# Performance work log

Measured on AMD Instinct MI355X. Metric: run time of the kernel, lower is better.

Reference implementation:

```python
import jax, jax.numpy as jnp
import numpy as np

B, IMG, TXT, DIM, H, D = 1, 1024, 256, 1536, 24, 64
SCALE = 1.0  # control cross-attn scale


def _lin(x, w, b):
    return x @ w + b


def _heads(x):  # [B,S,DIM] -> [B,H,S,D]
    return jnp.swapaxes(x.reshape(x.shape[0], x.shape[1], H, D), 1, 2)


def _merge(x):  # [B,H,S,D] -> [B,S,DIM]
    return jnp.swapaxes(x, 1, 2).reshape(x.shape[0], x.shape[2], H * D)


def _sdpa(q, k, v):
    s = jnp.einsum('bhqd,bhkd->bhqk', q, k) * (1.0 / np.sqrt(D))
    return jnp.einsum('bhqk,bhkd->bhqd', jax.nn.softmax(s, axis=-1), v)


def _rope(x, pe):  # x: [B,H,S,D], pe: [1,1,S,D//2,2,2]
    xr = x.reshape(*x.shape[:-1], -1, 1, 2)  # [B,H,S,D/2,1,2]
    out = pe[..., 0] * xr[..., 0] + pe[..., 1] * xr[..., 1]  # [B,H,S,D/2,2]
    return out.reshape(x.shape)


def _forward(hidden_states, encoder_hidden_states, hidden_states_control,
             encoder_hidden_states_control, img_to_q_control, pe,
             a_q_w, a_q_b, a_k_w, a_k_b, a_v_w, a_v_b,
             a_addq_w, a_addq_b, a_addk_w, a_addk_b, a_addv_w, a_addv_b,
             a_out_w, a_out_b, a_addout_w, a_addout_b,
             c_q_w, c_q_b, c_k_w, c_k_b, c_v_w, c_v_b,
             c_addq_w, c_addq_b, c_addk_w, c_addk_b, c_addv_w, c_addv_b,
             c_out_w, c_out_b, c_addout_w, c_addout_b):
    img_len = hidden_states.shape[1]
    # ---- main joint attention stream (no RoPE, per original) ----
    q = jnp.concatenate([_heads(_lin(hidden_states, a_q_w, a_q_b)),
                         _heads(_lin(encoder_hidden_states, a_addq_w, a_addq_b))], axis=2)
    k = jnp.concatenate([_heads(_lin(hidden_states, a_k_w, a_k_b)),
                         _heads(_lin(encoder_hidden_states, a_addk_w, a_addk_b))], axis=2)
    v = jnp.concatenate([_heads(_lin(hidden_states, a_v_w, a_v_b)),
                         _heads(_lin(encoder_hidden_states, a_addv_w, a_addv_b))], axis=2)
    hs = _merge(_sdpa(q, k, v))
    hs, ehs = hs[:, :img_len], hs[:, img_len:]
    # ---- control joint attention stream (with RoPE) ----
    qc = jnp.concatenate([_heads(_lin(hidden_states_control, c_q_w, c_q_b)),
                          _heads(_lin(encoder_hidden_states_control, c_addq_w, c_addq_b))], axis=2)
    kc = jnp.concatenate([_heads(_lin(hidden_states_control, c_k_w, c_k_b)),
                          _heads(_lin(encoder_hidden_states_control, c_addk_w, c_addk_b))], axis=2)
    vc = jnp.concatenate([_heads(_lin(hidden_states_control, c_v_w, c_v_b)),
                          _heads(_lin(encoder_hidden_states_control, c_addv_w, c_addv_b))], axis=2)
    key_cross, value_cross = kc, vc  # saved BEFORE RoPE, per original
    hsc = _merge(_sdpa(_rope(qc, pe), _rope(kc, pe), vc))
    hsc, ehsc = hsc[:, :img_len], hsc[:, img_len:]
    # ---- cross attention: img query attends to control K/V ----
    q_cross = _rope(_heads(img_to_q_control), pe[:, :, :img_len])
    k_cross = _rope(key_cross, pe[:, :, :key_cross.shape[2]])
    cross = _merge(_sdpa(q_cross, k_cross, value_cross))
    hs = hs + SCALE * cross
    # ---- output projections (to_out[1] is dropout p=0 -> identity) ----
    hs = _lin(hs, a_out_w, a_out_b)
    ehs = _lin(ehs, a_addout_w, a_addout_b)
    hsc = _lin(hsc, c_out_w, c_out_b)
    ehsc = _lin(ehsc, c_addout_w, c_addout_b)
    return hs, ehs, hsc, ehsc


def setup_inputs() -> dict:
    key = jax.random.key(0)
    ki = iter(jax.random.split(key, 80))
    d = {}
    d['hidden_states'] = jax.random.normal(next(ki), (B, IMG, DIM), jnp.float32)
    d['encoder_hidden_states'] = jax.random.normal(next(ki), (B, TXT, DIM), jnp.float32)
    d['hidden_states_control'] = jax.random.normal(next(ki), (B, IMG, DIM), jnp.float32)
    d['encoder_hidden_states_control'] = jax.random.normal(next(ki), (B, TXT, DIM), jnp.float32)
    d['img_to_q_control'] = jax.random.normal(next(ki), (B, IMG, DIM), jnp.float32)
    # realistic rotary pe: [1,1,S,D/2,2,2] rotation matrices
    S = IMG + TXT
    pos = np.arange(S, dtype=np.float32)
    freqs = 1.0 / (10000.0 ** (np.arange(0, D, 2, dtype=np.float32) / D))  # [D/2]
    ang = pos[:, None] * freqs[None, :]  # [S, D/2]
    cos, sin = np.cos(ang), np.sin(ang)
    pe = np.stack([np.stack([cos, -sin], -1), np.stack([sin, cos], -1)], -2)  # [S,D/2,2,2]
    d['pe'] = jnp.asarray(pe)[None, None]
    for p in ('a', 'c'):
        for name in ('q', 'k', 'v', 'addq', 'addk', 'addv', 'out', 'addout'):
            d[f'{p}_{name}_w'] = jax.random.normal(next(ki), (DIM, DIM), jnp.float32) * 0.02
            d[f'{p}_{name}_b'] = jax.random.normal(next(ki), (DIM,), jnp.float32) * 0.01
    return d


def reference(hidden_states, encoder_hidden_states, hidden_states_control,
              encoder_hidden_states_control, img_to_q_control, pe,
              a_q_w, a_q_b, a_k_w, a_k_b, a_v_w, a_v_b,
              a_addq_w, a_addq_b, a_addk_w, a_addk_b, a_addv_w, a_addv_b,
              a_out_w, a_out_b, a_addout_w, a_addout_b,
              c_q_w, c_q_b, c_k_w, c_k_b, c_v_w, c_v_b,
              c_addq_w, c_addq_b, c_addk_w, c_addk_b, c_addv_w, c_addv_b,
              c_out_w, c_out_b, c_addout_w, c_addout_b):
    return _forward(hidden_states, encoder_hidden_states, hidden_states_control,
                    encoder_hidden_states_control, img_to_q_control, pe,
                    a_q_w, a_q_b, a_k_w, a_k_b, a_v_w, a_v_b,
                    a_addq_w, a_addq_b, a_addk_w, a_addk_b, a_addv_w, a_addv_b,
                    a_out_w, a_out_b, a_addout_w, a_addout_b,
                    c_q_w, c_q_b, c_k_w, c_k_b, c_v_w, c_v_b,
                    c_addq_w, c_addq_b, c_addk_w, c_addk_b, c_addv_w, c_addv_b,
                    c_out_w, c_out_b, c_addout_w, c_addout_b)
```

## Files before the change

kernel.cpp:

```cpp
#include <hip/hip_runtime.h>

#define DIM 1536
#define IMG 1024
#define TXT 256
#define SEQ 1280
#define NH 24
#define HD 64
#define SD ((size_t)SEQ * DIM)
#define IDSZ ((size_t)IMG * DIM)

typedef __attribute__((ext_vector_type(8))) short short8;
typedef __attribute__((ext_vector_type(4))) float f32x4;

__device__ __forceinline__ float bf2f(ushort u) {
    union { unsigned int i; float f; } v; v.i = ((unsigned int)u) << 16; return v.f;
}
__device__ __forceinline__ ushort f2bf(float f) {
    union { unsigned int i; float f; } v; v.f = f;
    unsigned int u = v.i;
    u += 0x7fffu + ((u >> 16) & 1u);
    return (ushort)(u >> 16);
}

__global__ __launch_bounds__(256) void detect_dtype(const void* __restrict__ p,
                                                    int* __restrict__ flag)
{
    __shared__ int cnt;
    if (threadIdx.x == 0) cnt = 0;
    __syncthreads();
    const ushort* u = (const ushort*)p;
    int local = 0;
    for (int i = threadIdx.x; i < 2048; i += 256) {
        ushort v = u[2 * i];
        int e = (v >> 7) & 0xFF;
        if (e >= 0xC0) local++;
    }
    atomicAdd(&cnt, local);
    __syncthreads();
    if (threadIdx.x == 0) flag[0] = (cnt > 16) ? 1 : 0;
}

#define LSTR 40


struct QKV2P {
    const void* Xi[2]; const void* Xt[2];
    const void* W[12];
    const void* B[12];
    float* Y[6];
    ushort* Yh[6];
    ushort* Yl[6];
};

__global__ __launch_bounds__(256) void gemm_qkv_v3(QKV2P p, const int* __restrict__ dflag)
{
    __shared__ __align__(16) ushort As[2][128 * LSTR];
    __shared__ __align__(16) ushort Bs[2][64 * 64];
    const int dt = dflag[0];
    const int bx = blockIdx.x;
    const int wsel = bx / 12;
    const int n0 = (bx - wsel * 12) * 128;
    const int ys = blockIdx.y;
    const int str = (ys >= 10) ? 1 : 0;
    const int m0g = (ys - str * 10) * 128;
    const bool istxt = (m0g >= IMG);
    const int m0 = istxt ? (m0g - IMG) : m0g;
    const void* X  = istxt ? p.Xt[str] : p.Xi[str];
    const int widx = str * 6 + wsel + (istxt ? 3 : 0);
    const void* Wp = p.W[widx];
    const void* Bp = p.B[widx];
    const int yidx = str * 3 + wsel;
    float*  Y  = p.Y[yidx];
    ushort* yh = p.Yh[yidx];
    ushort* yl = p.Yl[yidx];

    const int t = threadIdx.x;
    const int wave = t >> 6, lane = t & 63;
    const int quad = lane >> 4, l16 = lane & 15;
    const int wm = (wave >> 1) * 64, wn = (wave & 1) * 64;

    const int arow = t >> 1, apair = t & 1;
    const int bn8 = (t & 15) << 3, bkk = (t >> 4) << 1;
    const int aps = apair ^ ((arow >> 3) & 1);
    const int adst = arow * LSTR + aps * 16;
    const int bkg = bkk >> 3, bo = bkk & 7;

    f32x4 acc[4][4];
#pragma unroll
    for (int i = 0; i < 4; ++i)
#pragma unroll
        for (int j = 0; j < 4; ++j) acc[i][j] = (f32x4)(0.0f);

    float4 raf[4]; uint4 rau[2];
    float4 rbf[4]; uint4 rbu[2];

    auto loadA = [&](int k0) {
        const size_t off = (size_t)(m0 + arow) * DIM + k0 + apair * 16;
        if (dt) {
            const float* xp = (const float*)X + off;
            raf[0] = *(const float4*)xp;       raf[1] = *(const float4*)(xp + 4);
            raf[2] = *(const float4*)(xp + 8); raf[3] = *(const float4*)(xp + 12);
        } else {
            const ushort* xp = (const ushort*)X + off;
            rau[0] = *(const uint4*)xp;
            rau[1] = *(const uint4*)(xp + 8);
        }
    };
    auto loadB = [&](int k0) {
        const size_t off = (size_t)(k0 + bkk) * DIM + n0 + bn8;
        if (dt) {
            const float* wp0 = (const float*)Wp + off;
            rbf[0] = *(const float4*)wp0;         rbf[1] = *(const float4*)(wp0 + 4);
            rbf[2] = *(const float4*)(wp0 + DIM); rbf[3] = *(const float4*)(wp0 + DIM + 4);
        } else {
            const ushort* wp0 = (const ushort*)Wp + off;
            rbu[0] = *(const uint4*)wp0;
            rbu[1] = *(const uint4*)(wp0 + DIM);
        }
    };
    auto storeA = [&](int buf) {
        ushort tmp[16];
        if (dt) {
            const float* xs = (const float*)raf;
#pragma unroll
            for (int i = 0; i < 16; ++i) tmp[i] = f2bf(xs[i]);
        } else {
            *(uint4*)&tmp[0] = rau[0];
            *(uint4*)&tmp[8] = rau[1];
        }
        *(uint4*)&As[buf][adst]     = *(uint4*)&tmp[0];
        *(uint4*)&As[buf][adst + 8] = *(uint4*)&tmp[8];
    };
    auto storeB = [&](int buf) {
        ushort t0[8], t1[8];
        if (dt) {
            const float* f = (const float*)rbf;
#pragma unroll
            for (int j = 0; j < 8; ++j) { t0[j] = f2bf(f[j]); t1[j] = f2bf(f[8 + j]); }
        } else {
            *(uint4*)t0 = rbu[0];
            *(uint4*)t1 = rbu[1];
        }
#pragma unroll
        for (int j = 0; j < 8; ++j) {
            const int rr = bn8 + j;
            const int R = rr & 63, half = rr >> 6;
            const int gx = (((half << 2) + bkg) ^ (R & 7) ^ (R >> 3)) & 7;
            *(unsigned int*)&Bs[buf][R * 64 + gx * 8 + bo] =
                (unsigned int)t0[j] | ((unsigned int)t1[j] << 16);
        }
    };

    loadA(0); loadB(0);
    storeA(0); storeB(0);
    __syncthreads();

    for (int k = 0; k < DIM / 32; ++k) {
        const int cur = k & 1;
        const bool hn = (k + 1) < DIM / 32;
        if (hn) { loadA((k + 1) * 32); loadB((k + 1) * 32); }

        short8 b[4];
#pragma unroll
        for (int j = 0; j < 4; ++j) {
            const int rrn = wn + j * 16 + l16;
            const int R = rrn & 63, half = rrn >> 6;
            const int gx = (((half << 2) + quad) ^ (R & 7) ^ (R >> 3)) & 7;
            b[j] = *(const short8*)&Bs[cur][R * 64 + gx * 8];
        }
#pragma unroll
        for (int i = 0; i < 4; ++i) {
            const int rr = wm + i * 16 + l16;
            const int ps = (quad >> 1) ^ ((rr >> 3) & 1);
            const int col = ps * 16 + (quad & 1) * 8;
            short8 a = *(const short8*)&As[cur][rr * LSTR + col];
#pragma unroll
            for (int j = 0; j < 4; ++j)
                acc[i][j] = __builtin_amdgcn_mfma_f32_16x16x32_bf16(a, b[j], acc[i][j], 0, 0, 0);
        }
        if (hn) { storeA(cur ^ 1); storeB(cur ^ 1); }
        __syncthreads();
    }

#pragma unroll
    for (int j = 0; j < 4; ++j) {
        const int col = n0 + wn + j * 16 + l16;
        const float bv = dt ? ((const float*)Bp)[col] : bf2f(((const ushort*)Bp)[col]);
#pragma unroll
        for (int i = 0; i < 4; ++i)
#pragma unroll
            for (int r = 0; r < 4; ++r) {
                const int row = m0g + wm + i * 16 + quad * 4 + r;
                const size_t o = (size_t)row * DIM + col;
                const float val = acc[i][j][r] + bv;
                if (Y) Y[o] = val;
                if (yh) {
                    const ushort hv = f2bf(val);
                    yh[o] = hv;
                    yl[o] = f2bf(val - bf2f(hv));
                }
            }
    }
}

struct OutP {
    const float* X;
    const void* W[4]; const void* B[4];
    void* out;
};

__global__ __launch_bounds__(256) void gemm_out_v3(OutP p, const int* __restrict__ dflag)
{
    __shared__ __align__(16) ushort Ah[2][64 * LSTR];
    __shared__ __align__(16) ushort Al[2][64 * LSTR];
    __shared__ __align__(16) ushort Bs[2][64 * 64];
    const int dt = dflag[0];
    const int n0 = blockIdx.x * 128;
    const int mt = blockIdx.y;
    const int seg = (mt < 16) ? 0 : (mt < 20) ? 1 : (mt < 36) ? 2 : 3;
    const void* Wp = p.W[seg];
    const void* Bp = p.B[seg];
    const int m0 = mt * 64;

    const int t = threadIdx.x;
    const int wave = t >> 6, lane = t & 63;
    const int quad = lane >> 4, l16 = lane & 15;
    const int wm = (wave >> 1) * 32, wn = (wave & 1) * 64;

    const int arow = t >> 2, ag = t & 3;
    const int apg = ag >> 1, asub = ag & 1;
    const int aps = apg ^ ((arow >> 3) & 1);
    const int adst = arow * LSTR + aps * 16 + asub * 8;
    const int bn8 = (t & 15) << 3, bkk = (t >> 4) << 1;
    const int bkg = bkk >> 3, bo = bkk & 7;

    f32x4 acc[2][4];
#pragma unroll
    for (int i = 0; i < 2; ++i)
#pragma unroll
        for (int j = 0; j < 4; ++j) acc[i][j] = (f32x4)(0.0f);

    float4 raf[2];
    float4 rbf[4]; uint4 rbu[2];

    auto loadA = [&](int k0) {
        const float* xp = p.X + (size_t)(m0 + arow) * DIM + k0 + ag * 8;
        raf[0] = *(const float4*)xp;
        raf[1] = *(const float4*)(xp + 4);
    };
    auto loadB = [&](int k0) {
        const size_t off = (size_t)(k0 + bkk) * DIM + n0 + bn8;
        if (dt) {
            const float* wp0 = (const float*)Wp + off;
            rbf[0] = *(const float4*)wp0;         rbf[1] = *(const float4*)(wp0 + 4);
            rbf[2] = *(const float4*)(wp0 + DIM); rbf[3] = *(const float4*)(wp0 + DIM + 4);
        } else {
            const ushort* wp0 = (const ushort*)Wp + off;
            rbu[0] = *(const uint4*)wp0;
            rbu[1] = *(const uint4*)(wp0 + DIM);
        }
    };
    auto storeA = [&](int buf) {
        ushort hi[8], lo[8];
        const float* xs = (const float*)raf;
#pragma unroll
        for (int i = 0; i < 8; ++i) {
            hi[i] = f2bf(xs[i]);
            lo[i] = f2bf(xs[i] - bf2f(hi[i]));
        }
        *(uint4*)&Ah[buf][adst] = *(uint4*)&hi[0];
        *(uint4*)&Al[buf][adst] = *(uint4*)&lo[0];
    };
    auto storeB = [&](int buf) {
        ushort t0[8], t1[8];
        if (dt) {
            const float* f = (const float*)rbf;
#pragma unroll
            for (int j = 0; j < 8; ++j) { t0[j] = f2bf(f[j]); t1[j] = f2bf(f[8 + j]); }
        } else {
            *(uint4*)t0 = rbu[0];
            *(uint4*)t1 = rbu[1];
        }
#pragma unroll
        for (int j = 0; j < 8; ++j) {
            const int rr = bn8 + j;
            const int R = rr & 63, half = rr >> 6;
            const int gx = (((half << 2) + bkg) ^ (R & 7) ^ (R >> 3)) & 7;
            *(unsigned int*)&Bs[buf][R * 64 + gx * 8 + bo] =
                (unsigned int)t0[j] | ((unsigned int)t1[j] << 16);
        }
    };

    loadA(0); loadB(0);
    storeA(0); storeB(0);
    __syncthreads();

    for (int k = 0; k < DIM / 32; ++k) {
        const int cur = k & 1;
        const bool hn = (k + 1) < DIM / 32;
        if (hn) { loadA((k + 1) * 32); loadB((k + 1) * 32); }

        short8 b[4];
#pragma unroll
        for (int j = 0; j < 4; ++j) {
            const int rrn = wn + j * 16 + l16;
            const int R = rrn & 63, half = rrn >> 6;
            const int gx = (((half << 2) + quad) ^ (R & 7) ^ (R >> 3)) & 7;
            b[j] = *(const short8*)&Bs[cur][R * 64 + gx * 8];
        }
#pragma unroll
        for (int i = 0; i < 2; ++i) {
            const int rr = wm + i * 16 + l16;
            const int ps = (quad >> 1) ^ ((rr >> 3) & 1);
            const int col = ps * 16 + (quad & 1) * 8;
            short8 ah = *(const short8*)&Ah[cur][rr * LSTR + col];
            short8 al = *(const short8*)&Al[cur][rr * LSTR + col];
#pragma unroll
            for (int j = 0; j < 4; ++j) {
                acc[i][j] = __builtin_amdgcn_mfma_f32_16x16x32_bf16(ah, b[j], acc[i][j], 0, 0, 0);
                acc[i][j] = __builtin_amdgcn_mfma_f32_16x16x32_bf16(al, b[j], acc[i][j], 0, 0, 0);
            }
        }
        if (hn) { storeA(cur ^ 1); storeB(cur ^ 1); }
        __syncthreads();
    }

#pragma unroll
    for (int j = 0; j < 4; ++j) {
        const int col = n0 + wn + j * 16 + l16;
        const float bv = dt ? ((const float*)Bp)[col] : bf2f(((const ushort*)Bp)[col]);
#pragma unroll
        for (int i = 0; i < 2; ++i)
#pragma unroll
            for (int r = 0; r < 4; ++r) {
                const int grow = m0 + wm + i * 16 + quad * 4 + r;
                const size_t o = (size_t)grow * DIM + col;
                const float val = acc[i][j][r] + bv;
                if (dt) ((float*)p.out)[o] = val;
                else    ((ushort*)p.out)[o] = f2bf(val);
            }
    }
}

__device__ __forceinline__ void pe_load(const void* pe, int dt, size_t off,
                                        float& c00, float& c01, float& c10, float& c11)
{
    if (dt) {
        float4 pv = *(const float4*)((const float*)pe + off);
        c00 = pv.x; c01 = pv.y; c10 = pv.z; c11 = pv.w;
    } else {
        const ushort* pp = (const ushort*)pe + off;
        c00 = bf2f(pp[0]); c01 = bf2f(pp[1]); c10 = bf2f(pp[2]); c11 = bf2f(pp[3]);
    }
}

__global__ __launch_bounds__(256) void rope_f32_to_split(
    const float* __restrict__ src, const void* __restrict__ pe,
    ushort* __restrict__ dh, ushort* __restrict__ dl,
    const int* __restrict__ dflag, int S)
{
    const int dt = dflag[0];
    int idx = blockIdx.x * 256 + threadIdx.x;
    if (idx >= S * 768) return;
    int s = idx / 768, pp = idx - s * 768;
    int col = pp << 1, i = pp & 31;
    float2 xv = *(const float2*)(src + (size_t)s * DIM + col);
    float c00, c01, c10, c11;
    pe_load(pe, dt, (size_t)s * 128 + i * 4, c00, c01, c10, c11);
    float y0 = c00 * xv.x + c01 * xv.y;
    float y1 = c10 * xv.x + c11 * xv.y;
    ushort h0 = f2bf(y0), h1 = f2bf(y1);
    ushort l0 = f2bf(y0 - bf2f(h0)), l1 = f2bf(y1 - bf2f(h1));
    *(unsigned int*)(dh + (size_t)s * DIM + col) = (unsigned int)h0 | ((unsigned int)h1 << 16);
    *(unsigned int*)(dl + (size_t)s * DIM + col) = (unsigned int)l0 | ((unsigned int)l1 << 16);
}

__global__ __launch_bounds__(256) void rope_in_to_split(
    const void* __restrict__ src, const void* __restrict__ pe,
    ushort* __restrict__ dh, ushort* __restrict__ dl,
    const int* __restrict__ dflag, int S)
{
    const int dt = dflag[0];
    int idx = blockIdx.x * 256 + threadIdx.x;
    if (idx >= S * 768) return;
    int s = idx / 768, pp = idx - s * 768;
    int col = pp << 1, i = pp & 31;
    float x0, x1;
    if (dt) {
        float2 xv = *(const float2*)((const float*)src + (size_t)s * DIM + col);
        x0 = xv.x; x1 = xv.y;
    } else {
        const ushort* sp = (const ushort*)src + (size_t)s * DIM + col;
        x0 = bf2f(sp[0]); x1 = bf2f(sp[1]);
    }
    float c00, c01, c10, c11;
    pe_load(pe, dt, (size_t)s * 128 + i * 4, c00, c01, c10, c11);
    float y0 = c00 * x0 + c01 * x1;
    float y1 = c10 * x0 + c11 * x1;
    ushort h0 = f2bf(y0), h1 = f2bf(y1);
    ushort l0 = f2bf(y0 - bf2f(h0)), l1 = f2bf(y1 - bf2f(h1));
    *(unsigned int*)(dh + (size_t)s * DIM + col) = (unsigned int)h0 | ((unsigned int)h1 << 16);
    *(unsigned int*)(dl + (size_t)s * DIM + col) = (unsigned int)l0 | ((unsigned int)l1 << 16);
}

__global__ __launch_bounds__(256) void vtrans_split(
    const float* __restrict__ V, ushort* __restrict__ Vth, ushort* __restrict__ Vtl,
    int seq)
{
    __shared__ unsigned int tile[64 * 65];
    const int s0 = blockIdx.x * 64;
    const int h = blockIdx.y;
    const int t = threadIdx.x;
#pragma unroll
    for (int it = 0; it < 16; ++it) {
        const int sl = (t >> 6) + (it << 2);
        const int d = t & 63;
        const float v = V[(size_t)(s0 + sl) * DIM + h * HD + d];
        const ushort hv = f2bf(v);
        const ushort lv = f2bf(v - bf2f(hv));
        tile[d * 65 + sl] = (unsigned int)hv | ((unsigned int)lv << 16);
    }
    __syncthreads();
    const int d = t >> 2, cc = (t & 3) << 4;
    ushort th[16], tl[16];
#pragma unroll
    for (int j = 0; j < 16; ++j) {
        const unsigned int w = tile[d * 65 + cc + j];
        th[j] = (ushort)w;
        tl[j] = (ushort)(w >> 16);
    }
    const size_t off = (size_t)(h * HD + d) * seq + s0 + cc;
    *(uint4*)(Vth + off)     = *(uint4*)&th[0];
    *(uint4*)(Vth + off + 8) = *(uint4*)&th[8];
    *(uint4*)(Vtl + off)     = *(uint4*)&tl[0];
    *(uint4*)(Vtl + off + 8) = *(uint4*)&tl[8];
}

__device__ __forceinline__ int swz(int row, int col) {
    return row * 64 + ((((col >> 3) ^ row) & 7) << 3) + (col & 7);
}
__device__ __forceinline__ short8 ldfrag(const ushort* plane, int row, int col) {
    return *(const short8*)&plane[swz(row, col)];
}

struct AttnP {
    const ushort *Qh, *Ql, *Kh, *Kl, *Vth, *Vtl;
    float* Op0;
    float* Op1;
    float2* Ml;
    int kvchunk;
    int kvstride;
};

__global__ __launch_bounds__(256) void attn_mfma_split(AttnP p)
{
    __shared__ ushort Qh_[4096], Ql_[4096];
    __shared__ ushort Kh_[4096], Kl_[4096];
    __shared__ ushort Vh_[4096], Vl_[4096];

    const int q0 = blockIdx.x * 64;
    const int h = blockIdx.y;
    const int z = blockIdx.z;
    const int t = threadIdx.x;
    const int wave = t >> 6, lane = t & 63;
    const int quad = lane >> 4, l16 = lane & 15;
    const int wq0 = wave * 16;

    const int srow = t >> 2, c0 = (t & 3) << 4;
    const int g0 = c0 >> 3;
    const int p0 = ((g0 ^ (srow & 7)) & 7) << 3;
    const int p1 = (((g0 + 1) ^ (srow & 7)) & 7) << 3;

    {
        const size_t off = (size_t)(q0 + srow) * DIM + h * HD + c0;
        *(uint4*)&Qh_[srow * 64 + p0] = *(const uint4*)(p.Qh + off);
        *(uint4*)&Qh_[srow * 64 + p1] = *(const uint4*)(p.Qh + off + 8);
        *(uint4*)&Ql_[srow * 64 + p0] = *(const uint4*)(p.Ql + off);
        *(uint4*)&Ql_[srow * 64 + p1] = *(const uint4*)(p.Ql + off + 8);
    }
    short8 qfh[2], qfl[2];
#pragma unroll
    for (int c = 0; c < 2; ++c) {
        qfh[c] = ldfrag(Qh_, wq0 + l16, c * 32 + quad * 8);
        qfl[c] = ldfrag(Ql_, wq0 + l16, c * 32 + quad * 8);
    }

    float m_[4], l_[4];
#pragma unroll
    for (int r = 0; r < 4; ++r) { m_[r] = -3e38f; l_[r] = 0.0f; }
    f32x4 Oacc[4];
#pragma unroll
    for (int j = 0; j < 4; ++j) Oacc[j] = (f32x4)(0.0f);

    const int kvbeg = z * p.kvchunk;
    for (int kt = 0; kt < p.kvchunk; kt += 64) {
        const int kv0 = kvbeg + kt;
        __syncthreads();
        {
            const size_t off = (size_t)(kv0 + srow) * DIM + h * HD + c0;
            *(uint4*)&Kh_[srow * 64 + p0] = *(const uint4*)(p.Kh + off);
            *(uint4*)&Kh_[srow * 64 + p1] = *(const uint4*)(p.Kh + off + 8);
            *(uint4*)&Kl_[srow * 64 + p0] = *(const uint4*)(p.Kl + off);
            *(uint4*)&Kl_[srow * 64 + p1] = *(const uint4*)(p.Kl + off + 8);
        }
        {
            const size_t off = (size_t)(h * HD + srow) * p.kvstride + kv0 + c0;
            *(uint4*)&Vh_[srow * 64 + p0] = *(const uint4*)(p.Vth + off);
            *(uint4*)&Vh_[srow * 64 + p1] = *(const uint4*)(p.Vth + off + 8);
            *(uint4*)&Vl_[srow * 64 + p0] = *(const uint4*)(p.Vtl + off);
            *(uint4*)&Vl_[srow * 64 + p1] = *(const uint4*)(p.Vtl + off + 8);
        }
        __syncthreads();

        f32x4 S[4];
#pragma unroll
        for (int j = 0; j < 4; ++j) S[j] = (f32x4)(0.0f);
#pragma unroll
        for (int c = 0; c < 2; ++c) {
#pragma unroll
            for (int j = 0; j < 4; ++j) {
                short8 bh = ldfrag(Kh_, j * 16 + l16, c * 32 + quad * 8);
                short8 bl = ldfrag(Kl_, j * 16 + l16, c * 32 + quad * 8);
                S[j] = __builtin_amdgcn_mfma_f32_16x16x32_bf16(qfh[c], bh, S[j], 0, 0, 0);
                S[j] = __builtin_amdgcn_mfma_f32_16x16x32_bf16(qfl[c], bh, S[j], 0, 0, 0);
                S[j] = __builtin_amdgcn_mfma_f32_16x16x32_bf16(qfh[c], bl, S[j], 0, 0, 0);
            }
        }
#pragma unroll
        for (int j = 0; j < 4; ++j)
#pragma unroll
            for (int r = 0; r < 4; ++r) S[j][r] *= 0.125f;

        float alpha[4];
#pragma unroll
        for (int r = 0; r < 4; ++r) {
            float mx = fmaxf(fmaxf(S[0][r], S[1][r]), fmaxf(S[2][r], S[3][r]));
            mx = fmaxf(mx, __shfl_xor(mx, 1));
            mx = fmaxf(mx, __shfl_xor(mx, 2));
            mx = fmaxf(mx, __shfl_xor(mx, 4));
            mx = fmaxf(mx, __shfl_xor(mx, 8));
            float mn = fmaxf(m_[r], mx);
            alpha[r] = __expf(m_[r] - mn);
            m_[r] = mn;
            float rs = 0.0f;
#pragma unroll
            for (int j = 0; j < 4; ++j) {
                float pv = __expf(S[j][r] - mn);
                S[j][r] = pv;
                rs += pv;
            }
            rs += __shfl_xor(rs, 1);
            rs += __shfl_xor(rs, 2);
            rs += __shfl_xor(rs, 4);
            rs += __shfl_xor(rs, 8);
            l_[r] = l_[r] * alpha[r] + rs;
        }
#pragma unroll
        for (int j = 0; j < 4; ++j)
#pragma unroll
            for (int r = 0; r < 4; ++r) Oacc[j][r] *= alpha[r];

        {
            const int prow = wq0 + quad * 4;
#pragma unroll
            for (int j = 0; j < 4; ++j)
#pragma unroll
                for (int r = 0; r < 4; ++r) {
                    float pv = S[j][r];
                    ushort ph = f2bf(pv);
                    ushort pl = f2bf(pv - bf2f(ph));
                    int idx = swz(prow + r, j * 16 + l16);
                    Qh_[idx] = ph;
                    Ql_[idx] = pl;
                }
        }

#pragma unroll
        for (int c = 0; c < 2; ++c) {
            short8 pah = ldfrag(Qh_, wq0 + l16, c * 32 + quad * 8);
            short8 pal = ldfrag(Ql_, wq0 + l16, c * 32 + quad * 8);
#pragma unroll
            for (int jn = 0; jn < 4; ++jn) {
                short8 vbh = ldfrag(Vh_, jn * 16 + l16, c * 32 + quad * 8);
                short8 vbl = ldfrag(Vl_, jn * 16 + l16, c * 32 + quad * 8);
                Oacc[jn] = __builtin_amdgcn_mfma_f32_16x16x32_bf16(pah, vbh, Oacc[jn], 0, 0, 0);
                Oacc[jn] = __builtin_amdgcn_mfma_f32_16x16x32_bf16(pal, vbh, Oacc[jn], 0, 0, 0);
                Oacc[jn] = __builtin_amdgcn_mfma_f32_16x16x32_bf16(pah, vbl, Oacc[jn], 0, 0, 0);
            }
        }
    }

    float* Opz = z ? p.Op1 : p.Op0;
#pragma unroll
    for (int r = 0; r < 4; ++r) {
        const int rowq = q0 + wq0 + quad * 4 + r;
        if (l16 == 0)
            p.Ml[((size_t)z * NH + h) * SEQ + rowq] = make_float2(m_[r], l_[r]);
#pragma unroll
        for (int jn = 0; jn < 4; ++jn)
            Opz[(size_t)rowq * DIM + h * HD + jn * 16 + l16] = Oacc[jn][r];
    }
}

__global__ __launch_bounds__(256) void attn_merge(
    const float* __restrict__ Op0, const float* __restrict__ Op1,
    const float2* __restrict__ Ml,
    float* __restrict__ out, const float* __restrict__ addto, int qlen)
{
    const int idx = blockIdx.x * 256 + threadIdx.x;
    if (idx >= qlen * 384) return;
    const int rowq = idx / 384;
    const int c4 = (idx - rowq * 384) << 2;
    const float2 a = Ml[(size_t)(c4 >> 6) * SEQ + rowq];
    const float2 b = Ml[(size_t)(NH + (c4 >> 6)) * SEQ + rowq];
    const float ms = fmaxf(a.x, b.x);
    const float s0 = __expf(a.x - ms), s1 = __expf(b.x - ms);
    const float inv = 1.0f / (s0 * a.y + s1 * b.y);
    const float4 o0 = *(const float4*)&Op0[(size_t)rowq * DIM + c4];
    const float4 o1 = *(const float4*)&Op1[(size_t)rowq * DIM + c4];
    float4 r;
    r.x = (s0 * o0.x + s1 * o1.x) * inv;
    r.y = (s0 * o0.y + s1 * o1.y) * inv;
    r.z = (s0 * o0.z + s1 * o1.z) * inv;
    r.w = (s0 * o0.w + s1 * o1.w) * inv;
    if (addto) {
        const float4 c = *(const float4*)&addto[(size_t)rowq * DIM + c4];
        r.x += c.x; r.y += c.y; r.z += c.z; r.w += c.w;
    }
    *(float4*)&out[(size_t)rowq * DIM + c4] = r;
}

extern "C" void kernel_launch(void* const* d_in, const int* in_sizes, int n_in,
                              void* d_out, int out_size, void* d_ws, size_t ws_size,
                              hipStream_t stream) {
    (void)in_sizes; (void)n_in; (void)out_size; (void)ws_size;
    const void* hs   = d_in[0];
    const void* ehs  = d_in[1];
    const void* hsc  = d_in[2];
    const void* ehsc = d_in[3];
    const void* i2q  = d_in[4];
    const void* pe   = d_in[5];
#define W_(i) ((const void*)d_in[i])

    int*   flag = (int*)d_ws;
    float* fb = (float*)((char*)d_ws + 256);
    float* q1 = fb;
    float* k1 = q1 + SD;
    float* v1 = k1 + SD;
    float* vC = v1 + SD;
    float* oA = vC + SD;
    float* oC = oA + SD;
    ushort* qh  = (ushort*)(oC + SD);
    ushort* qlo = qh + SD;
    ushort* kh  = qlo + SD;
    ushort* klo = kh + SD;
    ushort* vth = klo + SD;
    ushort* vtl = vth + SD;
    ushort* qxh = vtl + SD;
    ushort* qxl = qxh + IDSZ;
    float2* Ml = (float2*)(qxl + IDSZ);

    dim3 blk(256);
    detect_dtype<<<1, blk, 0, stream>>>(hs, flag);

    QKV2P qp;
    qp.Xi[0] = hs;  qp.Xt[0] = ehs;
    qp.Xi[1] = hsc; qp.Xt[1] = ehsc;
    for (int j = 0; j < 3; ++j) {
        qp.W[j]     = W_(6 + 2 * j);   qp.B[j]     = W_(7 + 2 * j);
        qp.W[3 + j] = W_(12 + 2 * j);  qp.B[3 + j] = W_(13 + 2 * j);
        qp.W[6 + j] = W_(22 + 2 * j);  qp.B[6 + j] = W_(23 + 2 * j);
        qp.W[9 + j] = W_(28 + 2 * j);  qp.B[9 + j] = W_(29 + 2 * j);
    }
    for (int j = 0; j < 6; ++j) { qp.Y[j] = nullptr; qp.Yh[j] = nullptr; qp.Yl[j] = nullptr; }
    qp.Yh[0] = qh;  qp.Yl[0] = qlo;
    qp.Yh[1] = kh;  qp.Yl[1] = klo;
    qp.Y[2] = v1;
    qp.Y[3] = q1;
    qp.Y[4] = k1;
    qp.Y[5] = vC;
    gemm_qkv_v3<<<dim3(36, 20), blk, 0, stream>>>(qp, flag);

    auto ATTN = [&](const ushort* Qhp, const ushort* Qlp, int qblocks,
                    float* Op0, float* Op1) {
        AttnP p;
        p.Qh = Qhp; p.Ql = Qlp;
        p.Kh = kh;  p.Kl = klo;
        p.Vth = vth; p.Vtl = vtl;
        p.Op0 = Op0; p.Op1 = Op1; p.Ml = Ml;
        p.kvchunk = SEQ / 2; p.kvstride = SEQ;
        attn_mfma_split<<<dim3(qblocks, NH, 2), blk, 0, stream>>>(p);
    };

    vtrans_split<<<dim3(SEQ / 64, NH), blk, 0, stream>>>(v1, vth, vtl, SEQ);
    ATTN(qh, qlo, SEQ / 64, v1, oC);
    attn_merge<<<(SEQ * 384 + 255) / 256, blk, 0, stream>>>(v1, oC, Ml, oA, nullptr, SEQ);

    rope_f32_to_split<<<(SEQ * 768 + 255) / 256, blk, 0, stream>>>(q1, pe, qh, qlo, flag, SEQ);
    rope_f32_to_split<<<(SEQ * 768 + 255) / 256, blk, 0, stream>>>(k1, pe, kh, klo, flag, SEQ);
    rope_in_to_split<<<(IMG * 768 + 255) / 256, blk, 0, stream>>>(i2q, pe, qxh, qxl, flag, IMG);
    vtrans_split<<<dim3(SEQ / 64, NH), blk, 0, stream>>>(vC, vth, vtl, SEQ);

    ATTN(qh, qlo, SEQ / 64, v1, oC);
    attn_merge<<<(SEQ * 384 + 255) / 256, blk, 0, stream>>>(v1, oC, Ml, oC, nullptr, SEQ);

    ATTN(qxh, qxl, IMG / 64, v1, vC);
    attn_merge<<<(IMG * 384 + 255) / 256, blk, 0, stream>>>(v1, vC, Ml, oA, oA, IMG);

    OutP op;
    op.X = oA;
    op.W[0] = W_(18); op.B[0] = W_(19);
    op.W[1] = W_(20); op.B[1] = W_(21);
    op.W[2] = W_(34); op.B[2] = W_(35);
    op.W[3] = W_(36); op.B[3] = W_(37);
    op.out = d_out;
    gemm_out_v3<<<dim3(12, 40), blk, 0, stream>>>(op, flag);
#undef W_
}
```

Baseline: 682.5 us.

## Pre-convert QKV weights and inputs to bf16; split Q inside attention

Adds a single batched conversion kernel that writes all twelve QKV weight matrices and the four activation inputs as bf16 into workspace. The QKV GEMM then reads only bf16 and no longer carries per-tile fp32 loads and conversion. Q is now stored as fp32 and split into hi/lo bf16 inside the attention kernel when it is loaded, so the separate Q split buffers go away and rope on Q runs in place. The cost is an extra full pass over the weights, about 28 MB of added bf16 writes and later reads, plus reshuffled workspace aliasing and higher attention Q-load traffic.

After: 654.9 us. 4.0% less time.

```diff
diff --git a/kernel.cpp b/kernel.cpp
--- a/kernel.cpp
+++ b/kernel.cpp
@@ -8,6 +8,7 @@
 #define HD 64
 #define SD ((size_t)SEQ * DIM)
 #define IDSZ ((size_t)IMG * DIM)
+#define WSZ ((size_t)DIM * DIM)
 
 typedef __attribute__((ext_vector_type(8))) short short8;
 typedef __attribute__((ext_vector_type(4))) float f32x4;
@@ -40,19 +41,45 @@
     if (threadIdx.x == 0) flag[0] = (cnt > 16) ? 1 : 0;
 }
 
+struct CvtP {
+    const void* src[16];
+    ushort* dst[16];
+    int n8[16];
+};
+
+__global__ __launch_bounds__(256) void convert_bf16(CvtP p, const int* __restrict__ dflag)
+{
+    const int a = blockIdx.y;
+    const int i = blockIdx.x * 256 + threadIdx.x;
+    if (i >= p.n8[a]) return;
+    const size_t off = (size_t)i * 8;
+    uint4 o;
+    if (dflag[0]) {
+        const float* s = (const float*)p.src[a] + off;
+        const float4 f0 = *(const float4*)s;
+        const float4 f1 = *(const float4*)(s + 4);
+        ushort t[8];
+        t[0] = f2bf(f0.x); t[1] = f2bf(f0.y); t[2] = f2bf(f0.z); t[3] = f2bf(f0.w);
+        t[4] = f2bf(f1.x); t[5] = f2bf(f1.y); t[6] = f2bf(f1.z); t[7] = f2bf(f1.w);
+        o = *(uint4*)t;
+    } else {
+        o = *(const uint4*)((const ushort*)p.src[a] + off);
+    }
+    *(uint4*)(p.dst[a] + off) = o;
+}
+
 #define LSTR 40
 
-
-struct QKV2P {
-    const void* Xi[2]; const void* Xt[2];
-    const void* W[12];
+struct QKV3P {
+    const ushort* Xb;
+    const ushort* Wb;
     const void* B[12];
     float* Y[6];
     ushort* Yh[6];
     ushort* Yl[6];
 };
 
-__global__ __launch_bounds__(256) void gemm_qkv_v3(QKV2P p, const int* __restrict__ dflag)
+__global__ __launch_bounds__(256) void gemm_qkv_v4(QKV3P p, const int* __restrict__ dflag)
 {
     __shared__ __align__(16) ushort As[2][128 * LSTR];
     __shared__ __align__(16) ushort Bs[2][64 * 64];
@@ -64,10 +91,9 @@
     const int str = (ys >= 10) ? 1 : 0;
     const int m0g = (ys - str * 10) * 128;
     const bool istxt = (m0g >= IMG);
-    const int m0 = istxt ? (m0g - IMG) : m0g;
-    const void* X  = istxt ? p.Xt[str] : p.Xi[str];
     const int widx = str * 6 + wsel + (istxt ? 3 : 0);
-    const void* Wp = p.W[widx];
+    const ushort* X  = p.Xb + (size_t)str * SD;
+    const ushort* Wp = p.Wb + (size_t)widx * WSZ;
     const void* Bp = p.B[widx];
     const int yidx = str * 3 + wsel;
     float*  Y  = p.Y[yidx];
@@ -91,56 +117,27 @@
 #pragma unroll
         for (int j = 0; j < 4; ++j) acc[i][j] = (f32x4)(0.0f);
 
-    float4 raf[4]; uint4 rau[2];
-    float4 rbf[4]; uint4 rbu[2];
+    uint4 rau[2];
+    uint4 rbu[2];
 
     auto loadA = [&](int k0) {
-        const size_t off = (size_t)(m0 + arow) * DIM + k0 + apair * 16;
-        if (dt) {
-            const float* xp = (const float*)X + off;
-            raf[0] = *(const float4*)xp;       raf[1] = *(const float4*)(xp + 4);
-            raf[2] = *(const float4*)(xp + 8); raf[3] = *(const float4*)(xp + 12);
-        } else {
-            const ushort* xp = (const ushort*)X + off;
-            rau[0] = *(const uint4*)xp;
-            rau[1] = *(const uint4*)(xp + 8);
-        }
+        const ushort* xp = X + (size_t)(m0g + arow) * DIM + k0 + apair * 16;
+        rau[0] = *(const uint4*)xp;
+        rau[1] = *(const uint4*)(xp + 8);
     };
     auto loadB = [&](int k0) {
-        const size_t off = (size_t)(k0 + bkk) * DIM + n0 + bn8;
-        if (dt) {
-            const float* wp0 = (const float*)Wp + off;
-            rbf[0] = *(const float4*)wp0;         rbf[1] = *(const float4*)(wp0 + 4);
-            rbf[2] = *(const float4*)(wp0 + DIM); rbf[3] = *(const float4*)(wp0 + DIM + 4);
-        } else {
-            const ushort* wp0 = (const ushort*)Wp + off;
-            rbu[0] = *(const uint4*)wp0;
-            rbu[1] = *(const uint4*)(wp0 + DIM);
-        }
+        const ushort* wp0 = Wp + (size_t)(k0 + bkk) * DIM + n0 + bn8;
+        rbu[0] = *(const uint4*)wp0;
+        rbu[1] = *(const uint4*)(wp0 + DIM);
     };
     auto storeA = [&](int buf) {
-        ushort tmp[16];
-        if (dt) {
-            const float* xs = (const float*)raf;
-#pragma unroll
-            for (int i = 0; i < 16; ++i) tmp[i] = f2bf(xs[i]);
-        } else {
-            *(uint4*)&tmp[0] = rau[0];
-            *(uint4*)&tmp[8] = rau[1];
-        }
-        *(uint4*)&As[buf][adst]     = *(uint4*)&tmp[0];
-        *(uint4*)&As[buf][adst + 8] = *(uint4*)&tmp[8];
+        *(uint4*)&As[buf][adst]     = rau[0];
+        *(uint4*)&As[buf][adst + 8] = rau[1];
     };
     auto storeB = [&](int buf) {
         ushort t0[8], t1[8];
-        if (dt) {
-            const float* f = (const float*)rbf;
-#pragma unroll
-            for (int j = 0; j < 8; ++j) { t0[j] = f2bf(f[j]); t1[j] = f2bf(f[8 + j]); }
-        } else {
-            *(uint4*)t0 = rbu[0];
-            *(uint4*)t1 = rbu[1];
-        }
+        *(uint4*)t0 = rbu[0];
+        *(uint4*)t1 = rbu[1];
 #pragma unroll
         for (int j = 0; j < 8; ++j) {
             const int rr = bn8 + j;
@@ -352,6 +349,23 @@
         const ushort* pp = (const ushort*)pe + off;
         c00 = bf2f(pp[0]); c01 = bf2f(pp[1]); c10 = bf2f(pp[2]); c11 = bf2f(pp[3]);
     }
+}
+
+__global__ __launch_bounds__(256) void rope_f32_inplace(
+    float* __restrict__ buf, const void* __restrict__ pe,
+    const int* __restrict__ dflag, int S)
+{
+    const int dt = dflag[0];
+    int idx = blockIdx.x * 256 + threadIdx.x;
+    if (idx >= S * 768) return;
+    int s = idx / 768, pp = idx - s * 768;
+    int col = pp << 1, i = pp & 31;
+    float* bp = buf + (size_t)s * DIM + col;
+    float x0 = bp[0], x1 = bp[1];
+    float c00, c01, c10, c11;
+    pe_load(pe, dt, (size_t)s * 128 + i * 4, c00, c01, c10, c11);
+    bp[0] = c00 * x0 + c01 * x1;
+    bp[1] = c10 * x0 + c11 * x1;
 }
 
 __global__ __launch_bounds__(256) void rope_f32_to_split(
@@ -375,10 +389,9 @@
     *(unsigned int*)(dl + (size_t)s * DIM + col) = (unsigned int)l0 | ((unsigned int)l1 << 16);
 }
 
-__global__ __launch_bounds__(256) void rope_in_to_split(
+__global__ __launch_bounds__(256) void rope_in_to_f32(
     const void* __restrict__ src, const void* __restrict__ pe,
-    ushort* __restrict__ dh, ushort* __restrict__ dl,
-    const int* __restrict__ dflag, int S)
+    float* __restrict__ dst, const int* __restrict__ dflag, int S)
 {
     const int dt = dflag[0];
     int idx = blockIdx.x * 256 + threadIdx.x;
@@ -395,12 +408,9 @@
     }
     float c00, c01, c10, c11;
     pe_load(pe, dt, (size_t)s * 128 + i * 4, c00, c01, c10, c11);
-    float y0 = c00 * x0 + c01 * x1;
-    float y1 = c10 * x0 + c11 * x1;
-    ushort h0 = f2bf(y0), h1 = f2bf(y1);
-    ushort l0 = f2bf(y0 - bf2f(h0)), l1 = f2bf(y1 - bf2f(h1));
-    *(unsigned int*)(dh + (size_t)s * DIM + col) = (unsigned int)h0 | ((unsigned int)h1 << 16);
-    *(unsigned int*)(dl + (size_t)s * DIM + col) = (unsigned int)l0 | ((unsigned int)l1 << 16);
+    float* dp = dst + (size_t)s * DIM + col;
+    dp[0] = c00 * x0 + c01 * x1;
+    dp[1] = c10 * x0 + c11 * x1;
 }
 
 __global__ __launch_bounds__(256) void vtrans_split(
@@ -444,7 +454,8 @@
 }
 
 struct AttnP {
-    const ushort *Qh, *Ql, *Kh, *Kl, *Vth, *Vtl;
+    const float* Qf;
+    const ushort *Kh, *Kl, *Vth, *Vtl;
     float* Op0;
     float* Op1;
     float2* Ml;
@@ -472,11 +483,22 @@
     const int p1 = (((g0 + 1) ^ (srow & 7)) & 7) << 3;
 
     {
-        const size_t off = (size_t)(q0 + srow) * DIM + h * HD + c0;
-        *(uint4*)&Qh_[srow * 64 + p0] = *(const uint4*)(p.Qh + off);
-        *(uint4*)&Qh_[srow * 64 + p1] = *(const uint4*)(p.Qh + off + 8);
-        *(uint4*)&Ql_[srow * 64 + p0] = *(const uint4*)(p.Ql + off);
-        *(uint4*)&Ql_[srow * 64 + p1] = *(const uint4*)(p.Ql + off + 8);
+        const float* src = p.Qf + (size_t)(q0 + srow) * DIM + h * HD + c0;
+        float x[16];
+        *(float4*)&x[0]  = *(const float4*)(src);
+        *(float4*)&x[4]  = *(const float4*)(src + 4);
+        *(float4*)&x[8]  = *(const float4*)(src + 8);
+        *(float4*)&x[12] = *(const float4*)(src + 12);
+        ushort hi[16], lo[16];
+#pragma unroll
+        for (int i = 0; i < 16; ++i) {
+            hi[i] = f2bf(x[i]);
+            lo[i] = f2bf(x[i] - bf2f(hi[i]));
+        }
+        *(uint4*)&Qh_[srow * 64 + p0] = *(uint4*)&hi[0];
+        *(uint4*)&Qh_[srow * 64 + p1] = *(uint4*)&hi[8];
+        *(uint4*)&Ql_[srow * 64 + p0] = *(uint4*)&lo[0];
+        *(uint4*)&Ql_[srow * 64 + p1] = *(uint4*)&lo[8];
     }
     short8 qfh[2], qfl[2];
 #pragma unroll
@@ -650,41 +672,53 @@
     float* vC = v1 + SD;
     float* oA = vC + SD;
     float* oC = oA + SD;
-    ushort* qh  = (ushort*)(oC + SD);
-    ushort* qlo = qh + SD;
-    ushort* kh  = qlo + SD;
+    ushort* kh  = (ushort*)(oC + SD);
     ushort* klo = kh + SD;
     ushort* vth = klo + SD;
     ushort* vtl = vth + SD;
-    ushort* qxh = vtl + SD;
-    ushort* qxl = qxh + IDSZ;
-    float2* Ml = (float2*)(qxl + IDSZ);
+    ushort* Wbf = vtl + SD;
+    ushort* Xbf = Wbf + 12 * WSZ;
+    float2* Ml = (float2*)(Xbf + 2 * SD);
+    float* qA = oC;
+    float* qx = k1;
 
     dim3 blk(256);
     detect_dtype<<<1, blk, 0, stream>>>(hs, flag);
 
-    QKV2P qp;
-    qp.Xi[0] = hs;  qp.Xt[0] = ehs;
-    qp.Xi[1] = hsc; qp.Xt[1] = ehsc;
-    for (int j = 0; j < 3; ++j) {
-        qp.W[j]     = W_(6 + 2 * j);   qp.B[j]     = W_(7 + 2 * j);
-        qp.W[3 + j] = W_(12 + 2 * j);  qp.B[3 + j] = W_(13 + 2 * j);
-        qp.W[6 + j] = W_(22 + 2 * j);  qp.B[6 + j] = W_(23 + 2 * j);
-        qp.W[9 + j] = W_(28 + 2 * j);  qp.B[9 + j] = W_(29 + 2 * j);
+    {
+        CvtP cp;
+        const int wsrc[12] = {6, 8, 10, 12, 14, 16, 22, 24, 26, 28, 30, 32};
+        for (int j = 0; j < 12; ++j) {
+            cp.src[j] = W_(wsrc[j]);
+            cp.dst[j] = Wbf + (size_t)j * WSZ;
+            cp.n8[j] = (int)(WSZ / 8);
+        }
+        cp.src[12] = hs;   cp.dst[12] = Xbf;                cp.n8[12] = (int)(IDSZ / 8);
+        cp.src[13] = ehs;  cp.dst[13] = Xbf + IDSZ;         cp.n8[13] = (int)((size_t)TXT * DIM / 8);
+        cp.src[14] = hsc;  cp.dst[14] = Xbf + SD;           cp.n8[14] = (int)(IDSZ / 8);
+        cp.src[15] = ehsc; cp.dst[15] = Xbf + SD + IDSZ;    cp.n8[15] = (int)((size_t)TXT * DIM / 8);
+        convert_bf16<<<dim3((int)(WSZ / 8 + 255) / 256, 16), blk, 0, stream>>>(cp, flag);
+    }
+
+    QKV3P qp;
+    qp.Xb = Xbf;
+    qp.Wb = Wbf;
+    {
+        const int bsrc[12] = {7, 9, 11, 13, 15, 17, 23, 25, 27, 29, 31, 33};
+        for (int j = 0; j < 12; ++j) qp.B[j] = W_(bsrc[j]);
     }
     for (int j = 0; j < 6; ++j) { qp.Y[j] = nullptr; qp.Yh[j] = nullptr; qp.Yl[j] = nullptr; }
-    qp.Yh[0] = qh;  qp.Yl[0] = qlo;
+    qp.Y[0] = qA;
     qp.Yh[1] = kh;  qp.Yl[1] = klo;
     qp.Y[2] = v1;
     qp.Y[3] = q1;
     qp.Y[4] = k1;
     qp.Y[5] = vC;
-    gemm_qkv_v3<<<dim3(36, 20), blk, 0, stream>>>(qp, flag);
-
-    auto ATTN = [&](const ushort* Qhp, const ushort* Qlp, int qblocks,
-                    float* Op0, float* Op1) {
+    gemm_qkv_v4<<<dim3(36, 20), blk, 0, stream>>>(qp, flag);
+
+    auto ATTN = [&](const float* Qfp, int qblocks, float* Op0, float* Op1) {
         AttnP p;
-        p.Qh = Qhp; p.Ql = Qlp;
+        p.Qf = Qfp;
         p.Kh = kh;  p.Kl = klo;
         p.Vth = vth; p.Vtl = vtl;
         p.Op0 = Op0; p.Op1 = Op1; p.Ml = Ml;
@@ -693,18 +727,18 @@
     };
 
     vtrans_split<<<dim3(SEQ / 64, NH), blk, 0, stream>>>(v1, vth, vtl, SEQ);
-    ATTN(qh, qlo, SEQ / 64, v1, oC);
-    attn_merge<<<(SEQ * 384 + 255) / 256, blk, 0, stream>>>(v1, oC, Ml, oA, nullptr, SEQ);
-
-    rope_f32_to_split<<<(SEQ * 768 + 255) / 256, blk, 0, stream>>>(q1, pe, qh, qlo, flag, SEQ);
+    ATTN(qA, SEQ / 64, v1, oA);
+    attn_merge<<<(SEQ * 384 + 255) / 256, blk, 0, stream>>>(v1, oA, Ml, oA, nullptr, SEQ);
+
+    rope_f32_inplace<<<(SEQ * 768 + 255) / 256, blk, 0, stream>>>(q1, pe, flag, SEQ);
     rope_f32_to_split<<<(SEQ * 768 + 255) / 256, blk, 0, stream>>>(k1, pe, kh, klo, flag, SEQ);
-    rope_in_to_split<<<(IMG * 768 + 255) / 256, blk, 0, stream>>>(i2q, pe, qxh, qxl, flag, IMG);
     vtrans_split<<<dim3(SEQ / 64, NH), blk, 0, stream>>>(vC, vth, vtl, SEQ);
-
-    ATTN(qh, qlo, SEQ / 64, v1, oC);
-    attn_merge<<<(SEQ * 384 + 255) / 256, blk, 0, stream>>>(v1, oC, Ml, oC, nullptr, SEQ);
-
-    ATTN(qxh, qxl, IMG / 64, v1, vC);
+    rope_in_to_f32<<<(IMG * 768 + 255) / 256, blk, 0, stream>>>(i2q, pe, qx, flag, IMG);
+
+    ATTN(q1, SEQ / 64, v1, vC);
+    attn_merge<<<(SEQ * 384 + 255) / 256, blk, 0, stream>>>(v1, vC, Ml, oC, nullptr, SEQ);
+
+    ATTN(qx, IMG / 64, v1, vC);
     attn_merge<<<(IMG * 384 + 255) / 256, blk, 0, stream>>>(v1, vC, Ml, oA, oA, IMG);
 
     OutP op;
```
